# Kernel optimization log

Measured on AMD Instinct MI355X. Metric: run time of the kernel, lower is better.

Reference implementation:

```python
import jax, jax.numpy as jnp
import numpy as np

D_MODEL = 2048
N_HEADS = 16
QK_ROPE = 64
QK_NOPE = 128
KV_LORA = 512
V_DIM = 128
QK_DIM = QK_ROPE + QK_NOPE
RMS_EPS = 1.1920928955078125e-07  # torch fp32 finfo.eps (nn.RMSNorm default eps=None)


def apply_rope(x, base=10000.0):
    # x: [B, S, H, D] ; torchtune-style interleaved-pair rotary
    B, S, H, D = x.shape
    freqs = 1.0 / (base ** (jnp.arange(0, D, 2, dtype=jnp.float32) / D))  # [D/2]
    t = jnp.arange(S, dtype=jnp.float32)[:, None] * freqs[None, :]        # [S, D/2]
    cos = jnp.cos(t)[None, :, None, :]
    sin = jnp.sin(t)[None, :, None, :]
    x1 = x[..., 0::2]
    x2 = x[..., 1::2]
    out = jnp.stack([x1 * cos - x2 * sin, x2 * cos + x1 * sin], axis=-1)
    return out.reshape(B, S, H, D).astype(x.dtype)


def setup_inputs() -> dict:
    key = jax.random.key(0)
    ks = jax.random.split(key, 6)
    s = lambda fan_in: 1.0 / np.sqrt(fan_in)
    x = jax.random.normal(ks[0], (2, 2048, D_MODEL), dtype=jnp.float32)
    Wq = jax.random.normal(ks[1], (D_MODEL, N_HEADS * QK_DIM), dtype=jnp.float32) * s(D_MODEL)
    Wkv_a = jax.random.normal(ks[2], (D_MODEL, KV_LORA + QK_ROPE), dtype=jnp.float32) * s(D_MODEL)
    kv_norm_w = jnp.ones((KV_LORA,), dtype=jnp.float32)
    Wkv_b = jax.random.normal(ks[3], (KV_LORA, N_HEADS * (QK_NOPE + V_DIM)), dtype=jnp.float32) * s(KV_LORA)
    Wo = jax.random.normal(ks[4], (N_HEADS * V_DIM, D_MODEL), dtype=jnp.float32) * s(N_HEADS * V_DIM)
    return {"x": x, "Wq": Wq, "Wkv_a": Wkv_a, "kv_norm_w": kv_norm_w, "Wkv_b": Wkv_b, "Wo": Wo}


def reference(x, Wq, Wkv_a, kv_norm_w, Wkv_b, Wo):
    B, S, _ = x.shape
    # queries: split nope/rope, rotary on rope slice only
    q = (x @ Wq).reshape(B, S, N_HEADS, QK_DIM)
    q_nope, q_rope = q[..., :QK_NOPE], q[..., QK_NOPE:]
    q = jnp.concatenate([q_nope, apply_rope(q_rope)], axis=-1)  # [B,S,H,QK_DIM]
    # compressed kv + decoupled rope key
    kv = x @ Wkv_a                                              # [B,S,KV_LORA+QK_ROPE]
    c_kv, k_rope = kv[..., :KV_LORA], kv[..., KV_LORA:]
    k_rope = apply_rope(k_rope.reshape(B, S, 1, QK_ROPE))       # [B,S,1,QK_ROPE]
    # RMSNorm on compressed latent, then decompress
    c_kv = c_kv * jax.lax.rsqrt(jnp.mean(c_kv * c_kv, axis=-1, keepdims=True) + RMS_EPS) * kv_norm_w
    kv = (c_kv @ Wkv_b).reshape(B, S, N_HEADS, QK_NOPE + V_DIM)
    k_nope, v = kv[..., :QK_NOPE], kv[..., QK_NOPE:]
    k = jnp.concatenate([k_nope, jnp.broadcast_to(k_rope, (B, S, N_HEADS, QK_ROPE))], axis=-1)
    # causal SDPA over sequence dim
    scale = 1.0 / np.sqrt(QK_DIM)
    scores = jnp.einsum('bqhd,bkhd->bhqk', q, k) * scale        # [B,H,S,S]
    mask = jnp.tril(jnp.ones((S, S), dtype=bool))
    scores = jnp.where(mask, scores, jnp.finfo(scores.dtype).min)
    attn = jax.nn.softmax(scores, axis=-1)
    out = jnp.einsum('bhqk,bkhd->bqhd', attn, v).reshape(B, S, N_HEADS * V_DIM)
    return out @ Wo
```

## Files before the change

### kernel.cpp

```cpp
#include <hip/hip_runtime.h>
#include <hip/hip_bf16.h>
#include <math.h>

#define BATCH   2
#define SEQ     2048
#define DM      2048
#define NH      16
#define QKR     64
#define QKN     128
#define KVL     512
#define VD      128
#define QKD     192
#define KVA_LD  640
#define RMS_EPS 1.1920928955078125e-07f

typedef __bf16 bf16x8 __attribute__((ext_vector_type(8)));
typedef float  f32x4  __attribute__((ext_vector_type(4)));

__device__ __forceinline__ void async16(const __bf16* g, __bf16* l)
{
    __builtin_amdgcn_global_load_lds(
        (__attribute__((address_space(1))) unsigned int*)g,
        (__attribute__((address_space(3))) unsigned int*)l,
        16, 0, 0);
}

template<int CTRL>
__device__ __forceinline__ float dppf(float x)
{
    int y = __builtin_amdgcn_update_dpp(0, __builtin_bit_cast(int, x), CTRL, 0xF, 0xF, false);
    return __builtin_bit_cast(float, y);
}

__global__ __launch_bounds__(256) void prep_kernel(const float* __restrict__ x,
                                                   __bf16* __restrict__ xb,
                                                   const float* __restrict__ Wq,
                                                   __bf16* __restrict__ Wq_t,
                                                   const float* __restrict__ Wkv_a,
                                                   __bf16* __restrict__ Wkva_t,
                                                   const float* __restrict__ Wkv_b,
                                                   __bf16* __restrict__ Wkvb_t,
                                                   const float* __restrict__ Wo,
                                                   __bf16* __restrict__ Wo_t)
{
    __shared__ float t[64][65];
    const int tid = threadIdx.x;
    int id = blockIdx.x;
    if (id < 8192) {
        int i = (id * 256 + tid) * 4;
        float4 v = *reinterpret_cast<const float4*>(x + i);
        xb[i + 0] = (__bf16)v.x;
        xb[i + 1] = (__bf16)v.y;
        xb[i + 2] = (__bf16)v.z;
        xb[i + 3] = (__bf16)v.w;
        return;
    }
    id -= 8192;
    const float* W; __bf16* Wt; int K, N, nb;
    if (id < 1536)      {            W = Wq;    Wt = Wq_t;   K = 2048; N = 3072; nb = 48; }
    else if (id < 1856) { id -= 1536; W = Wkv_a; Wt = Wkva_t; K = 2048; N = 576;  nb = 10; }
    else if (id < 2368) { id -= 1856; W = Wkv_b; Wt = Wkvb_t; K = 512;  N = 4096; nb = 64; }
    else                { id -= 2368; W = Wo;    Wt = Wo_t;   K = 2048; N = 2048; nb = 32; }
    const int n0 = (id % nb) * 64, k0 = (id / nb) * 64;
    #pragma unroll
    for (int i = 0; i < 16; ++i) {
        int flat = i * 256 + tid;
        int kl = flat >> 6, nl = flat & 63;
        t[kl][nl] = (n0 + nl < N) ? W[(size_t)(k0 + kl) * N + n0 + nl] : 0.f;
    }
    __syncthreads();
    #pragma unroll
    for (int i = 0; i < 16; ++i) {
        int flat = i * 256 + tid;
        int nl = flat >> 6, kl = flat & 63;
        Wt[(size_t)(n0 + nl) * K + k0 + kl] = (__bf16)t[kl][nl];
    }
}

template<typename OT>
__global__ __launch_bounds__(256) void gemm_bf16(const __bf16* __restrict__ A,
                                                 const __bf16* __restrict__ Bt,
                                                 OT* __restrict__ C,
                                                 int K, int lda, int ldb, int ldc)
{
    __shared__ __bf16 As[128 * 64];
    __shared__ __bf16 Bs[128 * 64];
    const int tid = threadIdx.x;
    const int lane = tid & 63, wave = tid >> 6;
    const int n = lane & 15, quad = lane >> 4;
    const int row0 = blockIdx.y * 128, col0 = blockIdx.x * 128;
    const int wm = (wave >> 1) * 64, wn = (wave & 1) * 64;

    f32x4 acc[4][4];
    #pragma unroll
    for (int mi = 0; mi < 4; ++mi)
        #pragma unroll
        for (int ni = 0; ni < 4; ++ni)
            #pragma unroll
            for (int r = 0; r < 4; ++r) acc[mi][ni][r] = 0.f;

    const int srow = tid >> 3;
    const int scol8p = tid & 7;
    const __bf16* Ag[4]; const __bf16* Bg[4];
    #pragma unroll
    for (int i = 0; i < 4; ++i) {
        int row = srow + i * 32;
        int col8l = scol8p ^ (row & 7);
        Ag[i] = A  + (size_t)(row0 + row) * lda + col8l * 8;
        Bg[i] = Bt + (size_t)(col0 + row) * ldb + col8l * 8;
    }
    __bf16* Asd = As + tid * 8;
    __bf16* Bsd = Bs + tid * 8;

    for (int k0 = 0; k0 < K; k0 += 64) {
        __syncthreads();
        #pragma unroll
        for (int i = 0; i < 4; ++i) {
            async16(Ag[i] + k0, Asd + i * 2048);
            async16(Bg[i] + k0, Bsd + i * 2048);
        }
        __syncthreads();

        #pragma unroll
        for (int kc = 0; kc < 2; ++kc) {
            bf16x8 af[4], bfr[4];
            #pragma unroll
            for (int mi = 0; mi < 4; ++mi) {
                int row = wm + mi * 16 + n;
                int slot = (kc * 4 + quad) ^ (row & 7);
                af[mi] = *reinterpret_cast<const bf16x8*>(&As[row * 64 + slot * 8]);
            }
            #pragma unroll
            for (int ni = 0; ni < 4; ++ni) {
                int row = wn + ni * 16 + n;
                int slot = (kc * 4 + quad) ^ (row & 7);
                bfr[ni] = *reinterpret_cast<const bf16x8*>(&Bs[row * 64 + slot * 8]);
            }
            #pragma unroll
            for (int mi = 0; mi < 4; ++mi)
                #pragma unroll
                for (int ni = 0; ni < 4; ++ni)
                    acc[mi][ni] = __builtin_amdgcn_mfma_f32_16x16x32_bf16(af[mi], bfr[ni], acc[mi][ni], 0, 0, 0);
        }
    }

    #pragma unroll
    for (int mi = 0; mi < 4; ++mi)
        #pragma unroll
        for (int r = 0; r < 4; ++r) {
            OT* cp = C + (size_t)(row0 + wm + mi * 16 + quad * 4 + r) * ldc + col0 + wn + n;
            #pragma unroll
            for (int ni = 0; ni < 4; ++ni)
                cp[ni * 16] = (OT)acc[mi][ni][r];
        }
}

__global__ __launch_bounds__(256) void post1_kernel(__bf16* __restrict__ q,
                                                    const float* __restrict__ kva,
                                                    const float* __restrict__ w,
                                                    __bf16* __restrict__ ckv,
                                                    __bf16* __restrict__ krope)
{
    const int tid = threadIdx.x;
    int id = blockIdx.x;
    if (id < 8192) {
        int idx = id * 256 + tid;
        int i = idx & 31;
        int h = (idx >> 5) & 15;
        int s = (idx >> 9) & 2047;
        int b = idx >> 20;
        float t = (float)s * __expf(-(float)(2 * i) / 64.0f * 9.210340371976184f);
        float c = __cosf(t), sn = __sinf(t);
        __bf16* p = q + ((size_t)(b * SEQ + s)) * (NH * QKD) + h * QKD + QKN + 2 * i;
        float x1 = (float)p[0], x2 = (float)p[1];
        p[0] = (__bf16)(x1 * c - x2 * sn);
        p[1] = (__bf16)(x2 * c + x1 * sn);
        return;
    }
    if (id < 8704) {
        int idx = (id - 8192) * 256 + tid;
        int i = idx & 31;
        int s = (idx >> 5) & 2047;
        int b = idx >> 16;
        float t = (float)s * __expf(-(float)(2 * i) / 64.0f * 9.210340371976184f);
        float c = __cosf(t), sn = __sinf(t);
        const float* p = kva + ((size_t)(b * SEQ + s)) * KVA_LD + KVL + 2 * i;
        float x1 = p[0], x2 = p[1];
        __bf16* o = krope + ((size_t)(b * SEQ + s)) * QKR + 2 * i;
        o[0] = (__bf16)(x1 * c - x2 * sn);
        o[1] = (__bf16)(x2 * c + x1 * sn);
        return;
    }
    const int rid = id - 8704;
    const float* row = kva + (size_t)rid * KVA_LD;
    float v[2];
    float ss = 0.f;
    #pragma unroll
    for (int j = 0; j < 2; ++j) {
        int d = tid + j * 256;
        v[j] = row[d];
        ss += v[j] * v[j];
    }
    #pragma unroll
    for (int off = 32; off > 0; off >>= 1) ss += __shfl_down(ss, off, 64);
    __shared__ float red[4];
    if ((tid & 63) == 0) red[tid >> 6] = ss;
    __syncthreads();
    float total = red[0] + red[1] + red[2] + red[3];
    float scale = 1.0f / sqrtf(total * (1.0f / KVL) + RMS_EPS);
    #pragma unroll
    for (int j = 0; j < 2; ++j) {
        int d = tid + j * 256;
        ckv[(size_t)rid * KVL + d] = (__bf16)(v[j] * scale * w[d]);
    }
}

__global__ __launch_bounds__(256) void build_vt(const __bf16* __restrict__ kvb,
                                                __bf16* __restrict__ Vt)
{
    __shared__ __bf16 tile[64][136];
    const int s0 = blockIdx.x * 64, h = blockIdx.y, b = blockIdx.z;
    const int t = threadIdx.x;
    #pragma unroll
    for (int i = 0; i < 4; ++i) {
        int flat = i * 256 + t;
        int sl = flat >> 4, c8 = flat & 15;
        bf16x8 v = *reinterpret_cast<const bf16x8*>(
            &kvb[((size_t)(b * SEQ + s0 + sl)) * (NH * 256) + h * 256 + 128 + c8 * 8]);
        *reinterpret_cast<bf16x8*>(&tile[sl][c8 * 8]) = v;
    }
    __syncthreads();
    #pragma unroll
    for (int j = 0; j < 32; ++j) {
        int flat = j * 256 + t;
        int d = flat >> 6, sl = flat & 63;
        Vt[((size_t)((b * NH + h) * VD + d)) * SEQ + s0 + sl] = tile[sl][d];
    }
}

#define LKS 200
#define LVS 72
#define LPS 72
__global__ __launch_bounds__(256, 2) void attn_mfma(const __bf16* __restrict__ qb,
                                                    const __bf16* __restrict__ kvb,
                                                    const __bf16* __restrict__ krope,
                                                    const __bf16* __restrict__ Vt,
                                                    __bf16* __restrict__ ob)
{
    __shared__ __bf16 Ks[64 * LKS];
    __shared__ __bf16 Vs[128 * LVS];
    __shared__ __bf16 Ps[8 * 16 * LPS];
    const int tid = threadIdx.x;
    const int wave = tid >> 6, lane = tid & 63;
    const int n = lane & 15, quad = lane >> 4;
    const int pair = blockIdx.x, h = blockIdx.y, b = blockIdx.z;
    const int bh = b * NH + h;
    const float scale = 0.07216878364870323f;
    const int qs1 = 31 - pair;
    const int mystrip = (wave >> 1) ? qs1 : pair;
    const int whalf = wave & 1;
    const int ntmax = qs1 + 1;

    const __bf16 one_bf = (__bf16)1.0f;
    const bf16x8 onesf = {one_bf, one_bf, one_bf, one_bf, one_bf, one_bf, one_bf, one_bf};

    bf16x8 qfrag[2][6];
    #pragma unroll
    for (int qt = 0; qt < 2; ++qt) {
        const int qrow = mystrip * 64 + whalf * 32 + qt * 16 + n;
        const __bf16* qp = qb + ((size_t)(b * SEQ + qrow)) * (NH * QKD) + h * QKD + quad * 8;
        #pragma unroll
        for (int c = 0; c < 6; ++c)
            qfrag[qt][c] = *reinterpret_cast<const bf16x8*>(qp + c * 32);
    }

    f32x4 Oa[2][8];
    f32x4 Ol[2];
    float m_i[2][4];
    #pragma unroll
    for (int qt = 0; qt < 2; ++qt) {
        #pragma unroll
        for (int i = 0; i < 8; ++i)
            #pragma unroll
            for (int r = 0; r < 4; ++r) Oa[qt][i][r] = 0.f;
        #pragma unroll
        for (int r = 0; r < 4; ++r) { Ol[qt][r] = 0.f; m_i[qt][r] = -1e30f; }
    }

    int kkey[6], kc8[6];
    #pragma unroll
    for (int i = 0; i < 6; ++i) {
        int flat = i * 256 + tid;
        kkey[i] = flat / 24; kc8[i] = flat % 24;
    }
    const int vd = tid >> 3, vc8 = tid & 7;

    const __bf16* Vg = Vt + (size_t)bh * VD * SEQ;

    bf16x8 kpre[6], vpre[4];
    {
        const int k0 = 0;
        #pragma unroll
        for (int i = 0; i < 6; ++i) {
            const __bf16* src = (kc8[i] < 16)
                ? kvb + ((size_t)(b * SEQ + k0 + kkey[i])) * (NH * 256) + h * 256 + kc8[i] * 8
                : krope + ((size_t)(b * SEQ + k0 + kkey[i])) * QKR + (kc8[i] - 16) * 8;
            kpre[i] = *reinterpret_cast<const bf16x8*>(src);
        }
        #pragma unroll
        for (int i = 0; i < 4; ++i)
            vpre[i] = *reinterpret_cast<const bf16x8*>(Vg + (size_t)(vd + i * 32) * SEQ + k0 + vc8 * 8);
    }

    for (int kt = 0; kt < ntmax; ++kt) {
        __syncthreads();
        #pragma unroll
        for (int i = 0; i < 6; ++i)
            *reinterpret_cast<bf16x8*>(&Ks[kkey[i] * LKS + kc8[i] * 8]) = kpre[i];
        #pragma unroll
        for (int i = 0; i < 4; ++i)
            *reinterpret_cast<bf16x8*>(&Vs[(vd + i * 32) * LVS + vc8 * 8]) = vpre[i];
        __syncthreads();

        if (kt + 1 < ntmax) {
            const int k0n = (kt + 1) * 64;
            #pragma unroll
            for (int i = 0; i < 6; ++i) {
                const __bf16* src = (kc8[i] < 16)
                    ? kvb + ((size_t)(b * SEQ + k0n + kkey[i])) * (NH * 256) + h * 256 + kc8[i] * 8
                    : krope + ((size_t)(b * SEQ + k0n + kkey[i])) * QKR + (kc8[i] - 16) * 8;
                kpre[i] = *reinterpret_cast<const bf16x8*>(src);
            }
            #pragma unroll
            for (int i = 0; i < 4; ++i)
                vpre[i] = *reinterpret_cast<const bf16x8*>(Vg + (size_t)(vd + i * 32) * SEQ + k0n + vc8 * 8);
        }

        if (kt <= mystrip) {
            const int k0 = kt * 64;

            f32x4 sacc[2][4];
            #pragma unroll
            for (int qt = 0; qt < 2; ++qt)
                #pragma unroll
                for (int t = 0; t < 4; ++t)
                    #pragma unroll
                    for (int r = 0; r < 4; ++r) sacc[qt][t][r] = 0.f;
            #pragma unroll
            for (int t = 0; t < 4; ++t)
                #pragma unroll
                for (int c = 0; c < 6; ++c) {
                    bf16x8 kf = *reinterpret_cast<const bf16x8*>(&Ks[(t * 16 + n) * LKS + c * 32 + quad * 8]);
                    sacc[0][t] = __builtin_amdgcn_mfma_f32_16x16x32_bf16(qfrag[0][c], kf, sacc[0][t], 0, 0, 0);
                    sacc[1][t] = __builtin_amdgcn_mfma_f32_16x16x32_bf16(qfrag[1][c], kf, sacc[1][t], 0, 0, 0);
                }

            const bool diag = (kt == mystrip);
            #pragma unroll
            for (int qt = 0; qt < 2; ++qt) {
                const int qg = mystrip * 64 + whalf * 32 + qt * 16 + quad * 4;
                float mloc[4];
                #pragma unroll
                for (int r = 0; r < 4; ++r) mloc[r] = -1e30f;
                #pragma unroll
                for (int t = 0; t < 4; ++t) {
                    int key = k0 + t * 16 + n;
                    #pragma unroll
                    for (int r = 0; r < 4; ++r) {
                        float sv = sacc[qt][t][r] * scale;
                        if (diag) sv = (key <= qg + r) ? sv : -1e30f;
                        sacc[qt][t][r] = sv;
                        mloc[r] = fmaxf(mloc[r], sv);
                    }
                }
                #pragma unroll
                for (int r = 0; r < 4; ++r) mloc[r] = fmaxf(mloc[r], dppf<0x121>(mloc[r]));
                #pragma unroll
                for (int r = 0; r < 4; ++r) mloc[r] = fmaxf(mloc[r], dppf<0x122>(mloc[r]));
                #pragma unroll
                for (int r = 0; r < 4; ++r) mloc[r] = fmaxf(mloc[r], dppf<0x124>(mloc[r]));
                #pragma unroll
                for (int r = 0; r < 4; ++r) mloc[r] = fmaxf(mloc[r], dppf<0x128>(mloc[r]));

                float mnew[4];
                #pragma unroll
                for (int r = 0; r < 4; ++r) mnew[r] = fmaxf(m_i[qt][r], mloc[r]);
                int grow = __any((mnew[0] > m_i[qt][0]) || (mnew[1] > m_i[qt][1]) ||
                                 (mnew[2] > m_i[qt][2]) || (mnew[3] > m_i[qt][3]));
                if (grow) {
                    float alpha[4];
                    #pragma unroll
                    for (int r = 0; r < 4; ++r) alpha[r] = __expf(m_i[qt][r] - mnew[r]);
                    #pragma unroll
                    for (int i = 0; i < 8; ++i)
                        #pragma unroll
                        for (int r = 0; r < 4; ++r) Oa[qt][i][r] *= alpha[r];
                    #pragma unroll
                    for (int r = 0; r < 4; ++r) Ol[qt][r] *= alpha[r];
                }
                #pragma unroll
                for (int r = 0; r < 4; ++r) m_i[qt][r] = mnew[r];

                #pragma unroll
                for (int t = 0; t < 4; ++t)
                    #pragma unroll
                    for (int r = 0; r < 4; ++r) {
                        float p = __expf(sacc[qt][t][r] - m_i[qt][r]);
                        Ps[wave * 32 * LPS + (qt * 16 + quad * 4 + r) * LPS + t * 16 + n] = (__bf16)p;
                    }
            }

            __asm__ volatile("s_waitcnt lgkmcnt(0)" ::: "memory");

            #pragma unroll
            for (int kc = 0; kc < 2; ++kc) {
                bf16x8 pf0 = *reinterpret_cast<const bf16x8*>(&Ps[wave * 32 * LPS + n * LPS + kc * 32 + quad * 8]);
                bf16x8 pf1 = *reinterpret_cast<const bf16x8*>(&Ps[wave * 32 * LPS + (16 + n) * LPS + kc * 32 + quad * 8]);
                Ol[0] = __builtin_amdgcn_mfma_f32_16x16x32_bf16(pf0, onesf, Ol[0], 0, 0, 0);
                Ol[1] = __builtin_amdgcn_mfma_f32_16x16x32_bf16(pf1, onesf, Ol[1], 0, 0, 0);
                #pragma unroll
                for (int vt = 0; vt < 8; ++vt) {
                    bf16x8 vf = *reinterpret_cast<const bf16x8*>(&Vs[(vt * 16 + n) * LVS + kc * 32 + quad * 8]);
                    Oa[0][vt] = __builtin_amdgcn_mfma_f32_16x16x32_bf16(pf0, vf, Oa[0][vt], 0, 0, 0);
                    Oa[1][vt] = __builtin_amdgcn_mfma_f32_16x16x32_bf16(pf1, vf, Oa[1][vt], 0, 0, 0);
                }
            }
        }
    }

    #pragma unroll
    for (int qt = 0; qt < 2; ++qt)
        #pragma unroll
        for (int r = 0; r < 4; ++r) {
            float inv = 1.0f / Ol[qt][r];
            int row = mystrip * 64 + whalf * 32 + qt * 16 + quad * 4 + r;
            __bf16* op = ob + ((size_t)(b * SEQ + row)) * (NH * VD) + h * VD;
            #pragma unroll
            for (int vt = 0; vt < 8; ++vt)
                op[vt * 16 + n] = (__bf16)(Oa[qt][vt][r] * inv);
        }
}

extern "C" void kernel_launch(void* const* d_in, const int* in_sizes, int n_in,
                              void* d_out, int out_size, void* d_ws, size_t ws_size,
                              hipStream_t stream)
{
    const float* x         = (const float*)d_in[0];
    const float* Wq        = (const float*)d_in[1];
    const float* Wkv_a     = (const float*)d_in[2];
    const float* kv_norm_w = (const float*)d_in[3];
    const float* Wkv_b     = (const float*)d_in[4];
    const float* Wo        = (const float*)d_in[5];
    float* out = (float*)d_out;

    float* ws = (float*)d_ws;
    __bf16* q_bf   = (__bf16*)ws;
    float*  kv_a   = ws + 6291456;
    __bf16* kv_b   = (__bf16*)(ws + 8912896);
    float*  r3     = ws + 17301504;
    __bf16* xb     = (__bf16*)r3;
    __bf16* Vt     = (__bf16*)r3;
    float*  r4     = ws + 21495808;
    __bf16* Wq_t   = (__bf16*)r4;
    __bf16* Wkva_t = (__bf16*)(r4 + 3145728);
    __bf16* Wkvb_t = (__bf16*)(r4 + 3801088);
    __bf16* attn_o = (__bf16*)r4;
    __bf16* Wo_t   = (__bf16*)(ws + 27787264);
    __bf16* c_kv_n = (__bf16*)(ws + 29884416);
    __bf16* krope  = (__bf16*)(ws + 30932992);

    const int M = BATCH * SEQ;
    dim3 blk(256);

    prep_kernel<<<11584, blk, 0, stream>>>(x, xb, Wq, Wq_t, Wkv_a, Wkva_t,
                                           Wkv_b, Wkvb_t, Wo, Wo_t);

    gemm_bf16<__bf16><<<dim3(3072 / 128, M / 128), blk, 0, stream>>>(xb, Wq_t, q_bf, DM, DM, DM, NH * QKD);
    gemm_bf16<float><<<dim3(640 / 128, M / 128), blk, 0, stream>>>(xb, Wkva_t, kv_a, DM, DM, DM, KVA_LD);

    post1_kernel<<<12800, blk, 0, stream>>>(q_bf, kv_a, kv_norm_w, c_kv_n, krope);

    gemm_bf16<__bf16><<<dim3(4096 / 128, M / 128), blk, 0, stream>>>(c_kv_n, Wkvb_t, kv_b, KVL, KVL, KVL, NH * 256);

    build_vt<<<dim3(SEQ / 64, NH, BATCH), blk, 0, stream>>>(kv_b, Vt);

    attn_mfma<<<dim3(16, NH, BATCH), blk, 0, stream>>>(q_bf, kv_b, krope, Vt, attn_o);

    gemm_bf16<float><<<dim3(2048 / 128, M / 128), blk, 0, stream>>>(attn_o, Wo_t, out, NH * VD, NH * VD, NH * VD, DM);
}
```

Measured before the change: 487.4 us.

## Give every wave rows from both causal strips to balance per-wave work

Each block pairs query strip `pair` with strip `31-pair`. Before, waves 0-1 took the short strip and waves 2-3 the long one, so half the waves sat idle through most key tiles. Now each wave owns 16 rows from each strip. It computes both strips while the short strip is still live and only the long strip afterwards, which balances MFMA work across waves. The cost is branchier code with duplicated MFMA loops, possibly higher register use, and 16-row instead of 32-row K-fragment reuse per wave on the long tail.

```diff
diff --git a/kernel.cpp b/kernel.cpp
--- a/kernel.cpp
+++ b/kernel.cpp
@@ -256,35 +256,34 @@
     const int pair = blockIdx.x, h = blockIdx.y, b = blockIdx.z;
     const int bh = b * NH + h;
     const float scale = 0.07216878364870323f;
-    const int qs1 = 31 - pair;
-    const int mystrip = (wave >> 1) ? qs1 : pair;
-    const int whalf = wave & 1;
-    const int ntmax = qs1 + 1;
+    int qs[2];
+    qs[0] = pair; qs[1] = 31 - pair;
+    const int ntmax = qs[1] + 1;
 
     const __bf16 one_bf = (__bf16)1.0f;
     const bf16x8 onesf = {one_bf, one_bf, one_bf, one_bf, one_bf, one_bf, one_bf, one_bf};
 
     bf16x8 qfrag[2][6];
     #pragma unroll
-    for (int qt = 0; qt < 2; ++qt) {
-        const int qrow = mystrip * 64 + whalf * 32 + qt * 16 + n;
+    for (int s = 0; s < 2; ++s) {
+        const int qrow = qs[s] * 64 + wave * 16 + n;
         const __bf16* qp = qb + ((size_t)(b * SEQ + qrow)) * (NH * QKD) + h * QKD + quad * 8;
         #pragma unroll
         for (int c = 0; c < 6; ++c)
-            qfrag[qt][c] = *reinterpret_cast<const bf16x8*>(qp + c * 32);
+            qfrag[s][c] = *reinterpret_cast<const bf16x8*>(qp + c * 32);
     }
 
     f32x4 Oa[2][8];
     f32x4 Ol[2];
     float m_i[2][4];
     #pragma unroll
-    for (int qt = 0; qt < 2; ++qt) {
+    for (int s = 0; s < 2; ++s) {
         #pragma unroll
         for (int i = 0; i < 8; ++i)
             #pragma unroll
-            for (int r = 0; r < 4; ++r) Oa[qt][i][r] = 0.f;
-        #pragma unroll
-        for (int r = 0; r < 4; ++r) { Ol[qt][r] = 0.f; m_i[qt][r] = -1e30f; }
+            for (int r = 0; r < 4; ++r) Oa[s][i][r] = 0.f;
+        #pragma unroll
+        for (int r = 0; r < 4; ++r) { Ol[s][r] = 0.f; m_i[s][r] = -1e30f; }
     }
 
     int kkey[6], kc8[6];
@@ -336,16 +335,17 @@
                 vpre[i] = *reinterpret_cast<const bf16x8*>(Vg + (size_t)(vd + i * 32) * SEQ + k0n + vc8 * 8);
         }
 
-        if (kt <= mystrip) {
-            const int k0 = kt * 64;
-
-            f32x4 sacc[2][4];
-            #pragma unroll
-            for (int qt = 0; qt < 2; ++qt)
-                #pragma unroll
-                for (int t = 0; t < 4; ++t)
-                    #pragma unroll
-                    for (int r = 0; r < 4; ++r) sacc[qt][t][r] = 0.f;
+        const int k0 = kt * 64;
+        const bool live0 = (kt <= qs[0]);
+
+        f32x4 sacc[2][4];
+        #pragma unroll
+        for (int s = 0; s < 2; ++s)
+            #pragma unroll
+            for (int t = 0; t < 4; ++t)
+                #pragma unroll
+                for (int r = 0; r < 4; ++r) sacc[s][t][r] = 0.f;
+        if (live0) {
             #pragma unroll
             for (int t = 0; t < 4; ++t)
                 #pragma unroll
@@ -354,64 +354,76 @@
                     sacc[0][t] = __builtin_amdgcn_mfma_f32_16x16x32_bf16(qfrag[0][c], kf, sacc[0][t], 0, 0, 0);
                     sacc[1][t] = __builtin_amdgcn_mfma_f32_16x16x32_bf16(qfrag[1][c], kf, sacc[1][t], 0, 0, 0);
                 }
-
-            const bool diag = (kt == mystrip);
-            #pragma unroll
-            for (int qt = 0; qt < 2; ++qt) {
-                const int qg = mystrip * 64 + whalf * 32 + qt * 16 + quad * 4;
-                float mloc[4];
-                #pragma unroll
-                for (int r = 0; r < 4; ++r) mloc[r] = -1e30f;
-                #pragma unroll
-                for (int t = 0; t < 4; ++t) {
-                    int key = k0 + t * 16 + n;
+        } else {
+            #pragma unroll
+            for (int t = 0; t < 4; ++t)
+                #pragma unroll
+                for (int c = 0; c < 6; ++c) {
+                    bf16x8 kf = *reinterpret_cast<const bf16x8*>(&Ks[(t * 16 + n) * LKS + c * 32 + quad * 8]);
+                    sacc[1][t] = __builtin_amdgcn_mfma_f32_16x16x32_bf16(qfrag[1][c], kf, sacc[1][t], 0, 0, 0);
+                }
+        }
+
+        #pragma unroll
+        for (int s = 0; s < 2; ++s) {
+            if (s == 0 && !live0) continue;
+
+            const int qg = qs[s] * 64 + wave * 16 + quad * 4;
+            const bool diag = (kt == qs[s]);
+            float mloc[4];
+            #pragma unroll
+            for (int r = 0; r < 4; ++r) mloc[r] = -1e30f;
+            #pragma unroll
+            for (int t = 0; t < 4; ++t) {
+                int key = k0 + t * 16 + n;
+                #pragma unroll
+                for (int r = 0; r < 4; ++r) {
+                    float sv = sacc[s][t][r] * scale;
+                    if (diag) sv = (key <= qg + r) ? sv : -1e30f;
+                    sacc[s][t][r] = sv;
+                    mloc[r] = fmaxf(mloc[r], sv);
+                }
+            }
+            #pragma unroll
+            for (int r = 0; r < 4; ++r) mloc[r] = fmaxf(mloc[r], dppf<0x121>(mloc[r]));
+            #pragma unroll
+            for (int r = 0; r < 4; ++r) mloc[r] = fmaxf(mloc[r], dppf<0x122>(mloc[r]));
+            #pragma unroll
+            for (int r = 0; r < 4; ++r) mloc[r] = fmaxf(mloc[r], dppf<0x124>(mloc[r]));
+            #pragma unroll
+            for (int r = 0; r < 4; ++r) mloc[r] = fmaxf(mloc[r], dppf<0x128>(mloc[r]));
+
+            float mnew[4];
+            #pragma unroll
+            for (int r = 0; r < 4; ++r) mnew[r] = fmaxf(m_i[s][r], mloc[r]);
+            int grow = __any((mnew[0] > m_i[s][0]) || (mnew[1] > m_i[s][1]) ||
+                             (mnew[2] > m_i[s][2]) || (mnew[3] > m_i[s][3]));
+            if (grow) {
+                float alpha[4];
+                #pragma unroll
+                for (int r = 0; r < 4; ++r) alpha[r] = __expf(m_i[s][r] - mnew[r]);
+                #pragma unroll
+                for (int i = 0; i < 8; ++i)
                     #pragma unroll
-                    for (int r = 0; r < 4; ++r) {
-                        float sv = sacc[qt][t][r] * scale;
-                        if (diag) sv = (key <= qg + r) ? sv : -1e30f;
-                        sacc[qt][t][r] = sv;
-                        mloc[r] = fmaxf(mloc[r], sv);
-                    }
+                    for (int r = 0; r < 4; ++r) Oa[s][i][r] *= alpha[r];
+                #pragma unroll
+                for (int r = 0; r < 4; ++r) Ol[s][r] *= alpha[r];
+            }
+            #pragma unroll
+            for (int r = 0; r < 4; ++r) m_i[s][r] = mnew[r];
+
+            #pragma unroll
+            for (int t = 0; t < 4; ++t)
+                #pragma unroll
+                for (int r = 0; r < 4; ++r) {
+                    float p = __expf(sacc[s][t][r] - m_i[s][r]);
+                    Ps[wave * 32 * LPS + (s * 16 + quad * 4 + r) * LPS + t * 16 + n] = (__bf16)p;
                 }
-                #pragma unroll
-                for (int r = 0; r < 4; ++r) mloc[r] = fmaxf(mloc[r], dppf<0x121>(mloc[r]));
-                #pragma unroll
-                for (int r = 0; r < 4; ++r) mloc[r] = fmaxf(mloc[r], dppf<0x122>(mloc[r]));
-                #pragma unroll
-                for (int r = 0; r < 4; ++r) mloc[r] = fmaxf(mloc[r], dppf<0x124>(mloc[r]));
-                #pragma unroll
-                for (int r = 0; r < 4; ++r) mloc[r] = fmaxf(mloc[r], dppf<0x128>(mloc[r]));
-
-                float mnew[4];
-                #pragma unroll
-                for (int r = 0; r < 4; ++r) mnew[r] = fmaxf(m_i[qt][r], mloc[r]);
-                int grow = __any((mnew[0] > m_i[qt][0]) || (mnew[1] > m_i[qt][1]) ||
-                                 (mnew[2] > m_i[qt][2]) || (mnew[3] > m_i[qt][3]));
-                if (grow) {
-                    float alpha[4];
-                    #pragma unroll
-                    for (int r = 0; r < 4; ++r) alpha[r] = __expf(m_i[qt][r] - mnew[r]);
-                    #pragma unroll
-                    for (int i = 0; i < 8; ++i)
-                        #pragma unroll
-                        for (int r = 0; r < 4; ++r) Oa[qt][i][r] *= alpha[r];
-                    #pragma unroll
-                    for (int r = 0; r < 4; ++r) Ol[qt][r] *= alpha[r];
-                }
-                #pragma unroll
-                for (int r = 0; r < 4; ++r) m_i[qt][r] = mnew[r];
-
-                #pragma unroll
-                for (int t = 0; t < 4; ++t)
-                    #pragma unroll
-                    for (int r = 0; r < 4; ++r) {
-                        float p = __expf(sacc[qt][t][r] - m_i[qt][r]);
-                        Ps[wave * 32 * LPS + (qt * 16 + quad * 4 + r) * LPS + t * 16 + n] = (__bf16)p;
-                    }
-            }
-
-            __asm__ volatile("s_waitcnt lgkmcnt(0)" ::: "memory");
-
+        }
+
+        __asm__ volatile("s_waitcnt lgkmcnt(0)" ::: "memory");
+
+        if (live0) {
             #pragma unroll
             for (int kc = 0; kc < 2; ++kc) {
                 bf16x8 pf0 = *reinterpret_cast<const bf16x8*>(&Ps[wave * 32 * LPS + n * LPS + kc * 32 + quad * 8]);
@@ -425,19 +437,30 @@
                     Oa[1][vt] = __builtin_amdgcn_mfma_f32_16x16x32_bf16(pf1, vf, Oa[1][vt], 0, 0, 0);
                 }
             }
-        }
-    }
-
-    #pragma unroll
-    for (int qt = 0; qt < 2; ++qt)
+        } else {
+            #pragma unroll
+            for (int kc = 0; kc < 2; ++kc) {
+                bf16x8 pf1 = *reinterpret_cast<const bf16x8*>(&Ps[wave * 32 * LPS + (16 + n) * LPS + kc * 32 + quad * 8]);
+                Ol[1] = __builtin_amdgcn_mfma_f32_16x16x32_bf16(pf1, onesf, Ol[1], 0, 0, 0);
+                #pragma unroll
+                for (int vt = 0; vt < 8; ++vt) {
+                    bf16x8 vf = *reinterpret_cast<const bf16x8*>(&Vs[(vt * 16 + n) * LVS + kc * 32 + quad * 8]);
+                    Oa[1][vt] = __builtin_amdgcn_mfma_f32_16x16x32_bf16(pf1, vf, Oa[1][vt], 0, 0, 0);
+                }
+            }
+        }
+    }
+
+    #pragma unroll
+    for (int s = 0; s < 2; ++s)
         #pragma unroll
         for (int r = 0; r < 4; ++r) {
-            float inv = 1.0f / Ol[qt][r];
-            int row = mystrip * 64 + whalf * 32 + qt * 16 + quad * 4 + r;
+            float inv = 1.0f / Ol[s][r];
+            int row = qs[s] * 64 + wave * 16 + quad * 4 + r;
             __bf16* op = ob + ((size_t)(b * SEQ + row)) * (NH * VD) + h * VD;
             #pragma unroll
             for (int vt = 0; vt < 8; ++vt)
-                op[vt * 16 + n] = (__bf16)(Oa[qt][vt][r] * inv);
+                op[vt * 16 + n] = (__bf16)(Oa[s][vt][r] * inv);
         }
 }
 
```

Result: slower. 673.9 us (+38.3%).
